# Performance work log

Measured on AMD Instinct MI355X. Metric: run time of the kernel, lower is better.

## Reference

```python
import jax, jax.numpy as jnp
import numpy as np

N_NODES = 100000
N_EDGES = 1600000
DIMS = [128, 128, 128, 64]


def setup_inputs() -> dict:
    key = jax.random.key(0)
    ks = jax.random.split(key, 12)
    inp = {
        "features": jax.random.normal(ks[0], (N_NODES, DIMS[0]), dtype=jnp.float32),
        "src": jax.random.randint(ks[1], (N_EDGES,), 0, N_NODES, dtype=jnp.int64),
        "dst": jax.random.randint(ks[2], (N_EDGES,), 0, N_NODES, dtype=jnp.int64),
        "edge_weight": jax.random.uniform(ks[3], (N_EDGES,), dtype=jnp.float32),
    }
    # GraphConv weights (xavier-like scale) and biases per layer
    for i in range(3):
        fin, fout = DIMS[i], DIMS[i + 1]
        scale = (2.0 / (fin + fout)) ** 0.5
        inp[f"W{i}"] = jax.random.normal(ks[4 + i], (fin, fout), dtype=jnp.float32) * scale
        inp[f"b{i}"] = jnp.zeros((fout,), dtype=jnp.float32)
    return inp


def _graph_conv(h, W, b, src, dst, ew, out_norm, in_norm):
    # DGL GraphConv, norm='both', with per-edge weight (u_mul_e message).
    fin, fout = W.shape
    h = h * out_norm[:, None]
    if fin > fout:  # mult W first to reduce message width
        h = h @ W
    msg = h[src] * ew[:, None]                       # [E, d] irregular gather
    agg = jax.ops.segment_sum(msg, dst, num_segments=N_NODES)
    agg = agg * in_norm[:, None]
    if fin <= fout:
        agg = agg @ W
    return agg + b


def reference(features, src, dst, edge_weight, W0, b0, W1, b1, W2, b2):
    ones = jnp.ones((N_EDGES,), dtype=features.dtype)
    out_deg = jax.ops.segment_sum(ones, src, num_segments=N_NODES)
    in_deg = jax.ops.segment_sum(ones, dst, num_segments=N_NODES)
    out_norm = jnp.clip(out_deg, 1.0, None) ** -0.5
    in_norm = jnp.clip(in_deg, 1.0, None) ** -0.5
    h = features
    Ws = [(W0, b0), (W1, b1), (W2, b2)]
    for i, (W, b) in enumerate(Ws):
        h = _graph_conv(h, W, b, src, dst, edge_weight, out_norm, in_norm)
        if i < len(Ws) - 1:
            h = jax.nn.relu(h)
    return h
```

## Files before the change

### kernel.cpp

```cpp
#include <hip/hip_runtime.h>
#include <cstddef>
#include <cstdint>

typedef float f4 __attribute__((ext_vector_type(4)));
typedef unsigned long long u64;
typedef unsigned short u16;
typedef unsigned short u16x8 __attribute__((ext_vector_type(8)));
typedef short short8 __attribute__((ext_vector_type(8)));

__device__ __forceinline__ u64 ldnt8(const void* p) {
    return __builtin_nontemporal_load((const u64*)(p));
}
__device__ __forceinline__ u16 bfrn(float f) {
    unsigned u = __float_as_uint(f);
    return (u16)((u + 0x7FFFu + ((u >> 16) & 1u)) >> 16);
}
__device__ __forceinline__ float bl(unsigned w) { return __uint_as_float(w << 16); }
__device__ __forceinline__ float bh(unsigned w) { return __uint_as_float(w & 0xFFFF0000u); }


#define EPB 4096

__global__ void __launch_bounds__(256)
k_p1(const int* __restrict__ src, const int* __restrict__ dst,
     u16* __restrict__ lrank_s, u16* __restrict__ lrank_d,
     int* __restrict__ bh_s, int* __restrict__ bh_d, int NB, int E) {
    __shared__ int hs[512], hd[512];
    const int t = threadIdx.x, b = blockIdx.x;
    for (int i = t; i < NB; i += 256) { hs[i] = 0; hd[i] = 0; }
    __syncthreads();
    const int e0 = b * EPB;
    #pragma unroll
    for (int j = 0; j < 4; ++j) {
        const int e = e0 + j * 1024 + t * 4;
        if (e + 4 <= E) {
            const int4 d = *(const int4*)&dst[e];
            const int4 s = *(const int4*)&src[e];
            unsigned rd0 = atomicAdd(&hd[d.x >> 8], 1);
            unsigned rd1 = atomicAdd(&hd[d.y >> 8], 1);
            unsigned rd2 = atomicAdd(&hd[d.z >> 8], 1);
            unsigned rd3 = atomicAdd(&hd[d.w >> 8], 1);
            unsigned rs0 = atomicAdd(&hs[s.x >> 8], 1);
            unsigned rs1 = atomicAdd(&hs[s.y >> 8], 1);
            unsigned rs2 = atomicAdd(&hs[s.z >> 8], 1);
            unsigned rs3 = atomicAdd(&hs[s.w >> 8], 1);
            *(uint2*)&lrank_d[e] = make_uint2(rd0 | (rd1 << 16), rd2 | (rd3 << 16));
            *(uint2*)&lrank_s[e] = make_uint2(rs0 | (rs1 << 16), rs2 | (rs3 << 16));
        } else {
            for (int k = e; k < E && k < e + 4; ++k) {
                lrank_d[k] = (u16)atomicAdd(&hd[dst[k] >> 8], 1);
                lrank_s[k] = (u16)atomicAdd(&hs[src[k] >> 8], 1);
            }
        }
    }
    __syncthreads();
    for (int i = t; i < NB; i += 256) {
        bh_d[b * NB + i] = hd[i];
        bh_s[b * NB + i] = hs[i];
    }
}

__global__ void __launch_bounds__(512)
k_p2(int* __restrict__ bh_d, int* __restrict__ bh_s,
     int* __restrict__ cb_d, int* __restrict__ cb_s, int NB, int B1) {
    __shared__ int s[512];
    const int B = blockIdx.x, i = threadIdx.x;
    int* bh = blockIdx.y ? bh_s : bh_d;
    int* cb = blockIdx.y ? cb_s : cb_d;
    const int v = (i < B1) ? bh[i * NB + B] : 0;
    s[i] = v;
    __syncthreads();
    for (int off = 1; off < 512; off <<= 1) {
        const int x = (i >= off) ? s[i - off] : 0;
        __syncthreads();
        s[i] += x;
        __syncthreads();
    }
    if (i < B1) bh[i * NB + B] = s[i] - v;
    if (i == 511) cb[B] = s[511];
}

__global__ void __launch_bounds__(512)
k_p2b(const int* __restrict__ cb_d, const int* __restrict__ cb_s,
      int* __restrict__ bktb_d, int* __restrict__ bktb_s,
      int* __restrict__ row, int NB, int N, int E) {
    __shared__ int s[512];
    const int t = threadIdx.x;
    int v = (t < NB) ? cb_d[t] : 0;
    s[t] = v;
    __syncthreads();
    for (int off = 1; off < 512; off <<= 1) {
        const int x = (t >= off) ? s[t - off] : 0;
        __syncthreads();
        s[t] += x;
        __syncthreads();
    }
    if (t < NB) bktb_d[t] = s[t] - v;
    __syncthreads();
    v = (t < NB) ? cb_s[t] : 0;
    s[t] = v;
    __syncthreads();
    for (int off = 1; off < 512; off <<= 1) {
        const int x = (t >= off) ? s[t - off] : 0;
        __syncthreads();
        s[t] += x;
        __syncthreads();
    }
    if (t < NB) bktb_s[t] = s[t] - v;
    if (t == 0) row[N] = E;
}

__global__ void __launch_bounds__(256)
k_p3(const int* __restrict__ src, const int* __restrict__ dst,
     const float* __restrict__ ew,
     const u16* __restrict__ lrank_s, const u16* __restrict__ lrank_d,
     const int* __restrict__ bh_s, const int* __restrict__ bh_d,
     const int* __restrict__ bktb_s, const int* __restrict__ bktb_d,
     int* __restrict__ tdst, int2* __restrict__ tsw, int* __restrict__ tsrc,
     int NB, int E) {
    const int t = threadIdx.x, b = blockIdx.x;
    const int e0 = b * EPB;
    #pragma unroll
    for (int j = 0; j < 4; ++j) {
        const int e = e0 + j * 1024 + t * 4;
        if (e + 4 <= E) {
            const int4 d = *(const int4*)&dst[e];
            const int4 s = *(const int4*)&src[e];
            const f4   w = *(const f4*)&ew[e];
            const uint2 rd = *(const uint2*)&lrank_d[e];
            const uint2 rs = *(const uint2*)&lrank_s[e];
            const int dd[4] = {d.x, d.y, d.z, d.w};
            const int ss[4] = {s.x, s.y, s.z, s.w};
            const float ww[4] = {w.x, w.y, w.z, w.w};
            const int rrd[4] = {(int)(rd.x & 0xFFFF), (int)(rd.x >> 16),
                                (int)(rd.y & 0xFFFF), (int)(rd.y >> 16)};
            const int rrs[4] = {(int)(rs.x & 0xFFFF), (int)(rs.x >> 16),
                                (int)(rs.y & 0xFFFF), (int)(rs.y >> 16)};
            #pragma unroll
            for (int k = 0; k < 4; ++k) {
                const int Bd = dd[k] >> 8;
                const int posd = bktb_d[Bd] + bh_d[b * NB + Bd] + rrd[k];
                tdst[posd] = dd[k];
                tsw[posd] = make_int2(ss[k], __float_as_int(ww[k]));
                const int Bs = ss[k] >> 8;
                const int poss = bktb_s[Bs] + bh_s[b * NB + Bs] + rrs[k];
                tsrc[poss] = ss[k];
            }
        } else {
            for (int k = e; k < E && k < e + 4; ++k) {
                const int dv = dst[k], sv = src[k];
                const int Bd = dv >> 8;
                const int posd = bktb_d[Bd] + bh_d[b * NB + Bd] + (int)lrank_d[k];
                tdst[posd] = dv;
                tsw[posd] = make_int2(sv, __float_as_int(ew[k]));
                const int Bs = sv >> 8;
                const int poss = bktb_s[Bs] + bh_s[b * NB + Bs] + (int)lrank_s[k];
                tsrc[poss] = sv;
            }
        }
    }
}

__global__ void __launch_bounds__(256)
k_p4s(const int* __restrict__ tsrc, const int* __restrict__ bktb_s,
      const int* __restrict__ cb_s, float* __restrict__ onorm, int NB, int N) {
    __shared__ int cnt[256];
    const int B = blockIdx.x, t = threadIdx.x;
    cnt[t] = 0;
    __syncthreads();
    const int base = bktb_s[B], cb = cb_s[B];
    for (int i = t; i < cb; i += 256) atomicAdd(&cnt[tsrc[base + i] & 255], 1);
    __syncthreads();
    const int n = (B << 8) + t;
    if (n < N) {
        const int c = cnt[t];
        onorm[n] = rsqrtf((float)(c < 1 ? 1 : c));
    }
}

__global__ void __launch_bounds__(256)
k_p4d(const int* __restrict__ tdst, const int2* __restrict__ tsw,
      const int* __restrict__ bktb_d, const int* __restrict__ cb_d,
      const float* __restrict__ onorm, int* __restrict__ row,
      float* __restrict__ inorm, int2* __restrict__ csr, int NB, int N) {
    __shared__ int cnt[256], cnt2[256], lrow[256], sc[256];
    const int B = blockIdx.x, t = threadIdx.x;
    cnt[t] = 0; cnt2[t] = 0;
    __syncthreads();
    const int base = bktb_d[B], cb = cb_d[B];
    for (int i = t; i < cb; i += 256) atomicAdd(&cnt[tdst[base + i] & 255], 1);
    __syncthreads();
    const int v = cnt[t];
    sc[t] = v;
    __syncthreads();
    for (int off = 1; off < 256; off <<= 1) {
        const int x = (t >= off) ? sc[t - off] : 0;
        __syncthreads();
        sc[t] += x;
        __syncthreads();
    }
    const int excl = sc[t] - v;
    lrow[t] = excl;
    const int n = (B << 8) + t;
    if (n < N) {
        row[n] = base + excl;
        inorm[n] = rsqrtf((float)(v < 1 ? 1 : v));
    }
    __syncthreads();
    for (int i = t; i < cb; i += 256) {
        const int d = tdst[base + i] & 255;
        const int2 sw = tsw[base + i];
        const int r = atomicAdd(&cnt2[d], 1);
        const float coef = __int_as_float(sw.y) * onorm[sw.x];
        csr[base + lrow[d] + r] = make_int2(sw.x, __float_as_int(coef));
    }
}

__global__ void __launch_bounds__(256)
k_cvt(const float* __restrict__ in, u16* __restrict__ out, int n8) {
    const int i = blockIdx.x * blockDim.x + threadIdx.x;
    if (i < n8) {
        const f4 v0 = *(const f4*)(in + (size_t)i * 8);
        const f4 v1 = *(const f4*)(in + (size_t)i * 8 + 4);
        u16x8 r = {bfrn(v0.x), bfrn(v0.y), bfrn(v0.z), bfrn(v0.w),
                   bfrn(v1.x), bfrn(v1.y), bfrn(v1.z), bfrn(v1.w)};
        *(u16x8*)(out + (size_t)i * 8) = r;
    }
}

template <int LOGC>
__global__ void __launch_bounds__(256)
k_wcvt(const float* __restrict__ W, u16* __restrict__ Wt, int K) {
    const int idx = blockIdx.x * 256 + threadIdx.x;
    if (idx < (K << LOGC)) {
        const int k = idx >> LOGC;
        const int c = idx & ((1 << LOGC) - 1);
        Wt[(size_t)c * K + k] = bfrn(W[idx]);
    }
}

__global__ void __launch_bounds__(256)
k_agg128b(const u16* __restrict__ h, const int* __restrict__ row,
          const int2* __restrict__ csr, const float* __restrict__ inorm,
          u16* __restrict__ out, int N) {
    const int node = (int)((blockIdx.x * blockDim.x + threadIdx.x) >> 6);
    if (node >= N) return;
    const int lane = threadIdx.x & 63;
    const int q = lane >> 4;
    const int col = (lane & 15) * 8;
    int p = row[node];
    const int e = row[node + 1];
    float a0 = 0, a1 = 0, a2 = 0, a3 = 0, a4 = 0, a5 = 0, a6 = 0, a7 = 0;
    for (; p + 16 <= e; p += 16) {
        const u64 c0 = ldnt8(&csr[p + q]);
        const u64 c1 = ldnt8(&csr[p + 4 + q]);
        const u64 c2 = ldnt8(&csr[p + 8 + q]);
        const u64 c3 = ldnt8(&csr[p + 12 + q]);
        const uint4 w0 = *(const uint4*)(h + (size_t)(int)c0 * 128 + col);
        const uint4 w1 = *(const uint4*)(h + (size_t)(int)c1 * 128 + col);
        const uint4 w2 = *(const uint4*)(h + (size_t)(int)c2 * 128 + col);
        const uint4 w3 = *(const uint4*)(h + (size_t)(int)c3 * 128 + col);
        const float f0 = __int_as_float((int)(c0 >> 32));
        const float f1 = __int_as_float((int)(c1 >> 32));
        const float f2 = __int_as_float((int)(c2 >> 32));
        const float f3 = __int_as_float((int)(c3 >> 32));
        a0 = fmaf(f0, bl(w0.x), a0); a1 = fmaf(f0, bh(w0.x), a1);
        a2 = fmaf(f0, bl(w0.y), a2); a3 = fmaf(f0, bh(w0.y), a3);
        a4 = fmaf(f0, bl(w0.z), a4); a5 = fmaf(f0, bh(w0.z), a5);
        a6 = fmaf(f0, bl(w0.w), a6); a7 = fmaf(f0, bh(w0.w), a7);
        a0 = fmaf(f1, bl(w1.x), a0); a1 = fmaf(f1, bh(w1.x), a1);
        a2 = fmaf(f1, bl(w1.y), a2); a3 = fmaf(f1, bh(w1.y), a3);
        a4 = fmaf(f1, bl(w1.z), a4); a5 = fmaf(f1, bh(w1.z), a5);
        a6 = fmaf(f1, bl(w1.w), a6); a7 = fmaf(f1, bh(w1.w), a7);
        a0 = fmaf(f2, bl(w2.x), a0); a1 = fmaf(f2, bh(w2.x), a1);
        a2 = fmaf(f2, bl(w2.y), a2); a3 = fmaf(f2, bh(w2.y), a3);
        a4 = fmaf(f2, bl(w2.z), a4); a5 = fmaf(f2, bh(w2.z), a5);
        a6 = fmaf(f2, bl(w2.w), a6); a7 = fmaf(f2, bh(w2.w), a7);
        a0 = fmaf(f3, bl(w3.x), a0); a1 = fmaf(f3, bh(w3.x), a1);
        a2 = fmaf(f3, bl(w3.y), a2); a3 = fmaf(f3, bh(w3.y), a3);
        a4 = fmaf(f3, bl(w3.z), a4); a5 = fmaf(f3, bh(w3.z), a5);
        a6 = fmaf(f3, bl(w3.w), a6); a7 = fmaf(f3, bh(w3.w), a7);
    }
    for (; p + 8 <= e; p += 8) {
        const u64 c0 = ldnt8(&csr[p + q]);
        const u64 c1 = ldnt8(&csr[p + 4 + q]);
        const uint4 w0 = *(const uint4*)(h + (size_t)(int)c0 * 128 + col);
        const uint4 w1 = *(const uint4*)(h + (size_t)(int)c1 * 128 + col);
        const float f0 = __int_as_float((int)(c0 >> 32));
        const float f1 = __int_as_float((int)(c1 >> 32));
        a0 = fmaf(f0, bl(w0.x), a0); a1 = fmaf(f0, bh(w0.x), a1);
        a2 = fmaf(f0, bl(w0.y), a2); a3 = fmaf(f0, bh(w0.y), a3);
        a4 = fmaf(f0, bl(w0.z), a4); a5 = fmaf(f0, bh(w0.z), a5);
        a6 = fmaf(f0, bl(w0.w), a6); a7 = fmaf(f0, bh(w0.w), a7);
        a0 = fmaf(f1, bl(w1.x), a0); a1 = fmaf(f1, bh(w1.x), a1);
        a2 = fmaf(f1, bl(w1.y), a2); a3 = fmaf(f1, bh(w1.y), a3);
        a4 = fmaf(f1, bl(w1.z), a4); a5 = fmaf(f1, bh(w1.z), a5);
        a6 = fmaf(f1, bl(w1.w), a6); a7 = fmaf(f1, bh(w1.w), a7);
    }
    {
        const int i0 = p + q, i1 = p + 4 + q;
        if (i0 < e) {
            const u64 c = ldnt8(&csr[i0]);
            const uint4 w = *(const uint4*)(h + (size_t)(int)c * 128 + col);
            const float f = __int_as_float((int)(c >> 32));
            a0 = fmaf(f, bl(w.x), a0); a1 = fmaf(f, bh(w.x), a1);
            a2 = fmaf(f, bl(w.y), a2); a3 = fmaf(f, bh(w.y), a3);
            a4 = fmaf(f, bl(w.z), a4); a5 = fmaf(f, bh(w.z), a5);
            a6 = fmaf(f, bl(w.w), a6); a7 = fmaf(f, bh(w.w), a7);
        }
        if (i1 < e) {
            const u64 c = ldnt8(&csr[i1]);
            const uint4 w = *(const uint4*)(h + (size_t)(int)c * 128 + col);
            const float f = __int_as_float((int)(c >> 32));
            a0 = fmaf(f, bl(w.x), a0); a1 = fmaf(f, bh(w.x), a1);
            a2 = fmaf(f, bl(w.y), a2); a3 = fmaf(f, bh(w.y), a3);
            a4 = fmaf(f, bl(w.z), a4); a5 = fmaf(f, bh(w.z), a5);
            a6 = fmaf(f, bl(w.w), a6); a7 = fmaf(f, bh(w.w), a7);
        }
    }
    a0 += __shfl_xor(a0, 16); a1 += __shfl_xor(a1, 16);
    a2 += __shfl_xor(a2, 16); a3 += __shfl_xor(a3, 16);
    a4 += __shfl_xor(a4, 16); a5 += __shfl_xor(a5, 16);
    a6 += __shfl_xor(a6, 16); a7 += __shfl_xor(a7, 16);
    a0 += __shfl_xor(a0, 32); a1 += __shfl_xor(a1, 32);
    a2 += __shfl_xor(a2, 32); a3 += __shfl_xor(a3, 32);
    a4 += __shfl_xor(a4, 32); a5 += __shfl_xor(a5, 32);
    a6 += __shfl_xor(a6, 32); a7 += __shfl_xor(a7, 32);
    if (lane < 16) {
        const float nn = inorm[node];
        u16x8 r = {bfrn(a0 * nn), bfrn(a1 * nn), bfrn(a2 * nn), bfrn(a3 * nn),
                   bfrn(a4 * nn), bfrn(a5 * nn), bfrn(a6 * nn), bfrn(a7 * nn)};
        *(u16x8*)(out + (size_t)node * 128 + col) = r;
    }
}

__global__ void __launch_bounds__(256)
k_agg64b(const u16* __restrict__ h, const int* __restrict__ row,
         const int2* __restrict__ csr, const float* __restrict__ inorm,
         const float* __restrict__ bias, float* __restrict__ out, int N) {
    const int node = (int)((blockIdx.x * blockDim.x + threadIdx.x) >> 6);
    if (node >= N) return;
    const int lane = threadIdx.x & 63;
    const int oc = lane >> 3;
    const int col = (lane & 7) * 8;
    int p = row[node];
    const int e = row[node + 1];
    float a0 = 0, a1 = 0, a2 = 0, a3 = 0, a4 = 0, a5 = 0, a6 = 0, a7 = 0;
    for (; p + 16 <= e; p += 16) {
        const u64 c0 = ldnt8(&csr[p + oc]);
        const u64 c1 = ldnt8(&csr[p + 8 + oc]);
        const uint4 w0 = *(const uint4*)(h + (size_t)(int)c0 * 64 + col);
        const uint4 w1 = *(const uint4*)(h + (size_t)(int)c1 * 64 + col);
        const float f0 = __int_as_float((int)(c0 >> 32));
        const float f1 = __int_as_float((int)(c1 >> 32));
        a0 = fmaf(f0, bl(w0.x), a0); a1 = fmaf(f0, bh(w0.x), a1);
        a2 = fmaf(f0, bl(w0.y), a2); a3 = fmaf(f0, bh(w0.y), a3);
        a4 = fmaf(f0, bl(w0.z), a4); a5 = fmaf(f0, bh(w0.z), a5);
        a6 = fmaf(f0, bl(w0.w), a6); a7 = fmaf(f0, bh(w0.w), a7);
        a0 = fmaf(f1, bl(w1.x), a0); a1 = fmaf(f1, bh(w1.x), a1);
        a2 = fmaf(f1, bl(w1.y), a2); a3 = fmaf(f1, bh(w1.y), a3);
        a4 = fmaf(f1, bl(w1.z), a4); a5 = fmaf(f1, bh(w1.z), a5);
        a6 = fmaf(f1, bl(w1.w), a6); a7 = fmaf(f1, bh(w1.w), a7);
    }
    {
        const int i0 = p + oc, i1 = p + 8 + oc;
        if (i0 < e) {
            const u64 c = ldnt8(&csr[i0]);
            const uint4 w = *(const uint4*)(h + (size_t)(int)c * 64 + col);
            const float f = __int_as_float((int)(c >> 32));
            a0 = fmaf(f, bl(w.x), a0); a1 = fmaf(f, bh(w.x), a1);
            a2 = fmaf(f, bl(w.y), a2); a3 = fmaf(f, bh(w.y), a3);
            a4 = fmaf(f, bl(w.z), a4); a5 = fmaf(f, bh(w.z), a5);
            a6 = fmaf(f, bl(w.w), a6); a7 = fmaf(f, bh(w.w), a7);
        }
        if (i1 < e) {
            const u64 c = ldnt8(&csr[i1]);
            const uint4 w = *(const uint4*)(h + (size_t)(int)c * 64 + col);
            const float f = __int_as_float((int)(c >> 32));
            a0 = fmaf(f, bl(w.x), a0); a1 = fmaf(f, bh(w.x), a1);
            a2 = fmaf(f, bl(w.y), a2); a3 = fmaf(f, bh(w.y), a3);
            a4 = fmaf(f, bl(w.z), a4); a5 = fmaf(f, bh(w.z), a5);
            a6 = fmaf(f, bl(w.w), a6); a7 = fmaf(f, bh(w.w), a7);
        }
    }
    a0 += __shfl_xor(a0, 8);  a1 += __shfl_xor(a1, 8);
    a2 += __shfl_xor(a2, 8);  a3 += __shfl_xor(a3, 8);
    a4 += __shfl_xor(a4, 8);  a5 += __shfl_xor(a5, 8);
    a6 += __shfl_xor(a6, 8);  a7 += __shfl_xor(a7, 8);
    a0 += __shfl_xor(a0, 16); a1 += __shfl_xor(a1, 16);
    a2 += __shfl_xor(a2, 16); a3 += __shfl_xor(a3, 16);
    a4 += __shfl_xor(a4, 16); a5 += __shfl_xor(a5, 16);
    a6 += __shfl_xor(a6, 16); a7 += __shfl_xor(a7, 16);
    a0 += __shfl_xor(a0, 32); a1 += __shfl_xor(a1, 32);
    a2 += __shfl_xor(a2, 32); a3 += __shfl_xor(a3, 32);
    a4 += __shfl_xor(a4, 32); a5 += __shfl_xor(a5, 32);
    a6 += __shfl_xor(a6, 32); a7 += __shfl_xor(a7, 32);
    if (lane < 8) {
        const float nn = inorm[node];
        const f4 b0 = *(const f4*)(bias + col);
        const f4 b1 = *(const f4*)(bias + col + 4);
        f4 r0 = {a0 * nn + b0.x, a1 * nn + b0.y, a2 * nn + b0.z, a3 * nn + b0.w};
        f4 r1 = {a4 * nn + b1.x, a5 * nn + b1.y, a6 * nn + b1.z, a7 * nn + b1.w};
        *(f4*)(out + (size_t)node * 64 + col) = r0;
        *(f4*)(out + (size_t)node * 64 + col + 4) = r1;
    }
}

template <int COLS, bool RELU, bool BIAS>
__global__ void __launch_bounds__(256)
k_mgemm(const u16* __restrict__ A, const u16* __restrict__ Wt,
        const float* __restrict__ bias, u16* __restrict__ C, int N) {
    __shared__ u16 Wl[COLS][136];
    const int t = threadIdx.x;
    const int lane = t & 63;
    const int wave = t >> 6;
    #pragma unroll
    for (int i = 0; i < COLS / 16; ++i) {
        const int elem = (i * 256 + t) * 8;
        const int r = elem >> 7, c0 = elem & 127;
        *(short8*)&Wl[r][c0] = *(const short8*)(Wt + elem);
    }
    const int row0 = blockIdx.x * 64 + wave * 16;
    const int arow = min(row0 + (lane & 15), N - 1);
    const int koff = (lane >> 4) * 8;
    short8 a[4];
    #pragma unroll
    for (int kk = 0; kk < 4; ++kk)
        a[kk] = *(const short8*)(A + (size_t)arow * 128 + kk * 32 + koff);
    __syncthreads();

    f4 acc[COLS / 16];
    #pragma unroll
    for (int ct = 0; ct < COLS / 16; ++ct) acc[ct] = (f4){0.f, 0.f, 0.f, 0.f};

    #pragma unroll
    for (int ct = 0; ct < COLS / 16; ++ct) {
        #pragma unroll
        for (int kk = 0; kk < 4; ++kk) {
            const short8 b = *(const short8*)&Wl[ct * 16 + (lane & 15)][kk * 32 + koff];
            acc[ct] = __builtin_amdgcn_mfma_f32_16x16x32_bf16(a[kk], b, acc[ct], 0, 0, 0);
        }
    }

    #pragma unroll
    for (int ct = 0; ct < COLS / 16; ++ct) {
        const int c = ct * 16 + (lane & 15);
        const float bb = BIAS ? bias[c] : 0.f;
        #pragma unroll
        for (int r = 0; r < 4; ++r) {
            const int gr = row0 + (lane >> 4) * 4 + r;
            if (gr < N) {
                float v = acc[ct][r] + bb;
                if (RELU) v = v > 0.f ? v : 0.f;
                C[(size_t)gr * COLS + c] = bfrn(v);
            }
        }
    }
}

extern "C" void kernel_launch(void* const* d_in, const int* in_sizes, int n_in,
                              void* d_out, int out_size, void* d_ws, size_t ws_size,
                              hipStream_t stream) {
    const float* feat = (const float*)d_in[0];
    const int*   src  = (const int*)d_in[1];
    const int*   dst  = (const int*)d_in[2];
    const float* ew   = (const float*)d_in[3];
    const float* W0   = (const float*)d_in[4];
    const float* b0   = (const float*)d_in[5];
    const float* W1   = (const float*)d_in[6];
    const float* b1   = (const float*)d_in[7];
    const float* W2   = (const float*)d_in[8];
    const float* b2   = (const float*)d_in[9];
    float* out = (float*)d_out;

    const int N = in_sizes[0] / 128;
    const int E = in_sizes[1];
    const int NB = (N + 255) / 256;
    const int B1 = (E + EPB - 1) / EPB;

    uint8_t* wp = (uint8_t*)d_ws;
    auto alloc = [&](size_t bytes) {
        uint8_t* r = wp;
        wp += (bytes + 511) & ~(size_t)511;
        return r;
    };
    u16*   featb = (u16*)alloc((size_t)N * 128 * 2);
    u16*   Xb    = (u16*)alloc((size_t)N * 128 * 2);
    u16*   Yb    = (u16*)alloc((size_t)N * 128 * 2 + 65536);
    int2*  csr   = (int2*)alloc((size_t)E * 8);
    int*   row   = (int*)alloc((size_t)(N + 1) * 4);
    float* onorm = (float*)alloc((size_t)N * 4);
    float* inorm = (float*)alloc((size_t)N * 4);
    u16*   Wt0   = (u16*)alloc(128 * 128 * 2);
    u16*   Wt1   = (u16*)alloc(128 * 128 * 2);
    u16*   Wt2   = (u16*)alloc(128 * 64 * 2);

    uint8_t* xp = (uint8_t*)Xb;
    auto xalloc = [&](size_t bytes) {
        uint8_t* r = xp;
        xp += (bytes + 511) & ~(size_t)511;
        return r;
    };
    u16* lrank_d = (u16*)xalloc((size_t)E * 2);
    u16* lrank_s = (u16*)xalloc((size_t)E * 2);
    int* bh_d    = (int*)xalloc((size_t)B1 * NB * 4);
    int* bh_s    = (int*)xalloc((size_t)B1 * NB * 4);
    int* cb_d    = (int*)xalloc((size_t)NB * 4);
    int* cb_s    = (int*)xalloc((size_t)NB * 4);
    int* bktb_d  = (int*)xalloc((size_t)NB * 4);
    int* bktb_s  = (int*)xalloc((size_t)NB * 4);

    uint8_t* yp = (uint8_t*)Yb;
    auto yalloc = [&](size_t bytes) {
        uint8_t* r = yp;
        yp += (bytes + 511) & ~(size_t)511;
        return r;
    };
    int*  tdst = (int*)yalloc((size_t)E * 4);
    int2* tsw  = (int2*)yalloc((size_t)E * 8);
    int*  tsrc = (int*)yalloc((size_t)E * 4);
    u16*  Gb   = (u16*)Yb;

    k_cvt<<<(N * 128 / 8 + 255) / 256, 256, 0, stream>>>(feat, featb, N * 128 / 8);
    k_wcvt<7><<<64, 256, 0, stream>>>(W0, Wt0, 128);
    k_wcvt<7><<<64, 256, 0, stream>>>(W1, Wt1, 128);
    k_wcvt<6><<<32, 256, 0, stream>>>(W2, Wt2, 128);
    k_p1<<<B1, 256, 0, stream>>>(src, dst, lrank_s, lrank_d, bh_s, bh_d, NB, E);
    k_p2<<<dim3(NB, 2), 512, 0, stream>>>(bh_d, bh_s, cb_d, cb_s, NB, B1);
    k_p2b<<<1, 512, 0, stream>>>(cb_d, cb_s, bktb_d, bktb_s, row, NB, N, E);
    k_p3<<<B1, 256, 0, stream>>>(src, dst, ew, lrank_s, lrank_d, bh_s, bh_d,
                                 bktb_s, bktb_d, tdst, tsw, tsrc, NB, E);
    k_p4s<<<NB, 256, 0, stream>>>(tsrc, bktb_s, cb_s, onorm, NB, N);
    k_p4d<<<NB, 256, 0, stream>>>(tdst, tsw, bktb_d, cb_d, onorm, row, inorm,
                                  csr, NB, N);

    const int ab = (N + 3) / 4;
    const int gb = (N + 63) / 64;

    k_agg128b<<<ab, 256, 0, stream>>>(featb, row, csr, inorm, Yb, N);
    k_mgemm<128, true, true><<<gb, 256, 0, stream>>>(Yb, Wt0, b0, Xb, N);
    k_agg128b<<<ab, 256, 0, stream>>>(Xb, row, csr, inorm, Yb, N);
    k_mgemm<128, true, true><<<gb, 256, 0, stream>>>(Yb, Wt1, b1, Xb, N);
    k_mgemm<64, false, false><<<gb, 256, 0, stream>>>(Xb, Wt2, nullptr, Gb, N);
    k_agg64b<<<ab, 256, 0, stream>>>(Gb, row, csr, inorm, b2, out, N);
}
```

Measured before the change: 338.7 us.

## Recompute local ranks in scatter pass and pack dst byte into src word

The histogram pass no longer writes per-edge local ranks. The scatter pass recomputes them with shared-memory atomics and caches bucket bases in shared memory. The separate tdst array is dropped by packing the low byte of dst into the top 8 bits of the src index in tsw, and tsrc shrinks from int to one byte. The three weight-conversion kernels are merged into one launch, and the workspace buffers are reassigned. This cuts global traffic and launch count, but relies on atomic rank order within a block matching the order in k_p1 only in counts, and it assumes node ids fit in 24 bits.

```diff
diff --git a/kernel.cpp b/kernel.cpp
--- a/kernel.cpp
+++ b/kernel.cpp
@@ -5,6 +5,7 @@
 typedef float f4 __attribute__((ext_vector_type(4)));
 typedef unsigned long long u64;
 typedef unsigned short u16;
+typedef unsigned char u8;
 typedef unsigned short u16x8 __attribute__((ext_vector_type(8)));
 typedef short short8 __attribute__((ext_vector_type(8)));
 
@@ -23,11 +24,10 @@
 
 __global__ void __launch_bounds__(256)
 k_p1(const int* __restrict__ src, const int* __restrict__ dst,
-     u16* __restrict__ lrank_s, u16* __restrict__ lrank_d,
      int* __restrict__ bh_s, int* __restrict__ bh_d, int NB, int E) {
     __shared__ int hs[512], hd[512];
     const int t = threadIdx.x, b = blockIdx.x;
-    for (int i = t; i < NB; i += 256) { hs[i] = 0; hd[i] = 0; }
+    for (int i = t; i < 512; i += 256) { hs[i] = 0; hd[i] = 0; }
     __syncthreads();
     const int e0 = b * EPB;
     #pragma unroll
@@ -36,20 +36,18 @@
         if (e + 4 <= E) {
             const int4 d = *(const int4*)&dst[e];
             const int4 s = *(const int4*)&src[e];
-            unsigned rd0 = atomicAdd(&hd[d.x >> 8], 1);
-            unsigned rd1 = atomicAdd(&hd[d.y >> 8], 1);
-            unsigned rd2 = atomicAdd(&hd[d.z >> 8], 1);
-            unsigned rd3 = atomicAdd(&hd[d.w >> 8], 1);
-            unsigned rs0 = atomicAdd(&hs[s.x >> 8], 1);
-            unsigned rs1 = atomicAdd(&hs[s.y >> 8], 1);
-            unsigned rs2 = atomicAdd(&hs[s.z >> 8], 1);
-            unsigned rs3 = atomicAdd(&hs[s.w >> 8], 1);
-            *(uint2*)&lrank_d[e] = make_uint2(rd0 | (rd1 << 16), rd2 | (rd3 << 16));
-            *(uint2*)&lrank_s[e] = make_uint2(rs0 | (rs1 << 16), rs2 | (rs3 << 16));
+            atomicAdd(&hd[d.x >> 8], 1);
+            atomicAdd(&hd[d.y >> 8], 1);
+            atomicAdd(&hd[d.z >> 8], 1);
+            atomicAdd(&hd[d.w >> 8], 1);
+            atomicAdd(&hs[s.x >> 8], 1);
+            atomicAdd(&hs[s.y >> 8], 1);
+            atomicAdd(&hs[s.z >> 8], 1);
+            atomicAdd(&hs[s.w >> 8], 1);
         } else {
             for (int k = e; k < E && k < e + 4; ++k) {
-                lrank_d[k] = (u16)atomicAdd(&hd[dst[k] >> 8], 1);
-                lrank_s[k] = (u16)atomicAdd(&hs[src[k] >> 8], 1);
+                atomicAdd(&hd[dst[k] >> 8], 1);
+                atomicAdd(&hs[src[k] >> 8], 1);
             }
         }
     }
@@ -113,12 +111,19 @@
 __global__ void __launch_bounds__(256)
 k_p3(const int* __restrict__ src, const int* __restrict__ dst,
      const float* __restrict__ ew,
-     const u16* __restrict__ lrank_s, const u16* __restrict__ lrank_d,
      const int* __restrict__ bh_s, const int* __restrict__ bh_d,
      const int* __restrict__ bktb_s, const int* __restrict__ bktb_d,
-     int* __restrict__ tdst, int2* __restrict__ tsw, int* __restrict__ tsrc,
-     int NB, int E) {
+     int2* __restrict__ tsw, u8* __restrict__ tsrc, int NB, int E) {
+    __shared__ int hs[512], hd[512], base_s[512], base_d[512];
     const int t = threadIdx.x, b = blockIdx.x;
+    for (int i = t; i < 512; i += 256) {
+        hs[i] = 0; hd[i] = 0;
+        if (i < NB) {
+            base_d[i] = bktb_d[i] + bh_d[b * NB + i];
+            base_s[i] = bktb_s[i] + bh_s[b * NB + i];
+        }
+    }
+    __syncthreads();
     const int e0 = b * EPB;
     #pragma unroll
     for (int j = 0; j < 4; ++j) {
@@ -127,49 +132,43 @@
             const int4 d = *(const int4*)&dst[e];
             const int4 s = *(const int4*)&src[e];
             const f4   w = *(const f4*)&ew[e];
-            const uint2 rd = *(const uint2*)&lrank_d[e];
-            const uint2 rs = *(const uint2*)&lrank_s[e];
             const int dd[4] = {d.x, d.y, d.z, d.w};
             const int ss[4] = {s.x, s.y, s.z, s.w};
             const float ww[4] = {w.x, w.y, w.z, w.w};
-            const int rrd[4] = {(int)(rd.x & 0xFFFF), (int)(rd.x >> 16),
-                                (int)(rd.y & 0xFFFF), (int)(rd.y >> 16)};
-            const int rrs[4] = {(int)(rs.x & 0xFFFF), (int)(rs.x >> 16),
-                                (int)(rs.y & 0xFFFF), (int)(rs.y >> 16)};
             #pragma unroll
             for (int k = 0; k < 4; ++k) {
                 const int Bd = dd[k] >> 8;
-                const int posd = bktb_d[Bd] + bh_d[b * NB + Bd] + rrd[k];
-                tdst[posd] = dd[k];
-                tsw[posd] = make_int2(ss[k], __float_as_int(ww[k]));
+                const int rd = atomicAdd(&hd[Bd], 1);
+                tsw[base_d[Bd] + rd] = make_int2(ss[k] | ((dd[k] & 255) << 24),
+                                                 __float_as_int(ww[k]));
                 const int Bs = ss[k] >> 8;
-                const int poss = bktb_s[Bs] + bh_s[b * NB + Bs] + rrs[k];
-                tsrc[poss] = ss[k];
+                const int rs = atomicAdd(&hs[Bs], 1);
+                tsrc[base_s[Bs] + rs] = (u8)(ss[k] & 255);
             }
         } else {
             for (int k = e; k < E && k < e + 4; ++k) {
                 const int dv = dst[k], sv = src[k];
                 const int Bd = dv >> 8;
-                const int posd = bktb_d[Bd] + bh_d[b * NB + Bd] + (int)lrank_d[k];
-                tdst[posd] = dv;
-                tsw[posd] = make_int2(sv, __float_as_int(ew[k]));
+                const int rd = atomicAdd(&hd[Bd], 1);
+                tsw[base_d[Bd] + rd] = make_int2(sv | ((dv & 255) << 24),
+                                                 __float_as_int(ew[k]));
                 const int Bs = sv >> 8;
-                const int poss = bktb_s[Bs] + bh_s[b * NB + Bs] + (int)lrank_s[k];
-                tsrc[poss] = sv;
+                const int rs = atomicAdd(&hs[Bs], 1);
+                tsrc[base_s[Bs] + rs] = (u8)(sv & 255);
             }
         }
     }
 }
 
 __global__ void __launch_bounds__(256)
-k_p4s(const int* __restrict__ tsrc, const int* __restrict__ bktb_s,
+k_p4s(const u8* __restrict__ tsrc, const int* __restrict__ bktb_s,
       const int* __restrict__ cb_s, float* __restrict__ onorm, int NB, int N) {
     __shared__ int cnt[256];
     const int B = blockIdx.x, t = threadIdx.x;
     cnt[t] = 0;
     __syncthreads();
     const int base = bktb_s[B], cb = cb_s[B];
-    for (int i = t; i < cb; i += 256) atomicAdd(&cnt[tsrc[base + i] & 255], 1);
+    for (int i = t; i < cb; i += 256) atomicAdd(&cnt[tsrc[base + i]], 1);
     __syncthreads();
     const int n = (B << 8) + t;
     if (n < N) {
@@ -179,7 +178,7 @@
 }
 
 __global__ void __launch_bounds__(256)
-k_p4d(const int* __restrict__ tdst, const int2* __restrict__ tsw,
+k_p4d(const int2* __restrict__ tsw,
       const int* __restrict__ bktb_d, const int* __restrict__ cb_d,
       const float* __restrict__ onorm, int* __restrict__ row,
       float* __restrict__ inorm, int2* __restrict__ csr, int NB, int N) {
@@ -188,7 +187,8 @@
     cnt[t] = 0; cnt2[t] = 0;
     __syncthreads();
     const int base = bktb_d[B], cb = cb_d[B];
-    for (int i = t; i < cb; i += 256) atomicAdd(&cnt[tdst[base + i] & 255], 1);
+    for (int i = t; i < cb; i += 256)
+        atomicAdd(&cnt[((unsigned)tsw[base + i].x) >> 24], 1);
     __syncthreads();
     const int v = cnt[t];
     sc[t] = v;
@@ -208,11 +208,12 @@
     }
     __syncthreads();
     for (int i = t; i < cb; i += 256) {
-        const int d = tdst[base + i] & 255;
         const int2 sw = tsw[base + i];
+        const int d = ((unsigned)sw.x) >> 24;
+        const int s = sw.x & 0xFFFFFF;
         const int r = atomicAdd(&cnt2[d], 1);
-        const float coef = __int_as_float(sw.y) * onorm[sw.x];
-        csr[base + lrow[d] + r] = make_int2(sw.x, __float_as_int(coef));
+        const float coef = __int_as_float(sw.y) * onorm[s];
+        csr[base + lrow[d] + r] = make_int2(s, __float_as_int(coef));
     }
 }
 
@@ -228,14 +229,20 @@
     }
 }
 
-template <int LOGC>
-__global__ void __launch_bounds__(256)
-k_wcvt(const float* __restrict__ W, u16* __restrict__ Wt, int K) {
-    const int idx = blockIdx.x * 256 + threadIdx.x;
-    if (idx < (K << LOGC)) {
-        const int k = idx >> LOGC;
-        const int c = idx & ((1 << LOGC) - 1);
-        Wt[(size_t)c * K + k] = bfrn(W[idx]);
+__global__ void __launch_bounds__(256)
+k_wcvt3(const float* __restrict__ W0, const float* __restrict__ W1,
+        const float* __restrict__ W2, u16* __restrict__ Wt0,
+        u16* __restrict__ Wt1, u16* __restrict__ Wt2) {
+    const int i = blockIdx.x * 256 + threadIdx.x;
+    if (i < 16384) {
+        const int k = i >> 7, c = i & 127;
+        Wt0[c * 128 + k] = bfrn(W0[i]);
+    } else if (i < 32768) {
+        const int j = i - 16384, k = j >> 7, c = j & 127;
+        Wt1[c * 128 + k] = bfrn(W1[j]);
+    } else if (i < 40960) {
+        const int j = i - 32768, k = j >> 6, c = j & 63;
+        Wt2[c * 128 + k] = bfrn(W2[j]);
     }
 }
 
@@ -486,7 +493,8 @@
     };
     u16*   featb = (u16*)alloc((size_t)N * 128 * 2);
     u16*   Xb    = (u16*)alloc((size_t)N * 128 * 2);
-    u16*   Yb    = (u16*)alloc((size_t)N * 128 * 2 + 65536);
+    u16*   Tb    = (u16*)alloc((size_t)N * 128 * 2);
+    u8*    scr   = (u8*)alloc((size_t)E * 10 + 65536);
     int2*  csr   = (int2*)alloc((size_t)E * 8);
     int*   row   = (int*)alloc((size_t)(N + 1) * 4);
     float* onorm = (float*)alloc((size_t)N * 4);
@@ -501,46 +509,40 @@
         xp += (bytes + 511) & ~(size_t)511;
         return r;
     };
-    u16* lrank_d = (u16*)xalloc((size_t)E * 2);
-    u16* lrank_s = (u16*)xalloc((size_t)E * 2);
-    int* bh_d    = (int*)xalloc((size_t)B1 * NB * 4);
-    int* bh_s    = (int*)xalloc((size_t)B1 * NB * 4);
-    int* cb_d    = (int*)xalloc((size_t)NB * 4);
-    int* cb_s    = (int*)xalloc((size_t)NB * 4);
-    int* bktb_d  = (int*)xalloc((size_t)NB * 4);
-    int* bktb_s  = (int*)xalloc((size_t)NB * 4);
-
-    uint8_t* yp = (uint8_t*)Yb;
+    int* bh_d   = (int*)xalloc((size_t)B1 * NB * 4);
+    int* bh_s   = (int*)xalloc((size_t)B1 * NB * 4);
+    int* cb_d   = (int*)xalloc((size_t)NB * 4);
+    int* cb_s   = (int*)xalloc((size_t)NB * 4);
+    int* bktb_d = (int*)xalloc((size_t)NB * 4);
+    int* bktb_s = (int*)xalloc((size_t)NB * 4);
+
+    uint8_t* yp = scr;
     auto yalloc = [&](size_t bytes) {
         uint8_t* r = yp;
         yp += (bytes + 511) & ~(size_t)511;
         return r;
     };
-    int*  tdst = (int*)yalloc((size_t)E * 4);
     int2* tsw  = (int2*)yalloc((size_t)E * 8);
-    int*  tsrc = (int*)yalloc((size_t)E * 4);
-    u16*  Gb   = (u16*)Yb;
+    u8*   tsrc = (u8*)yalloc((size_t)E);
+    u16*  Gb   = (u16*)scr;
 
     k_cvt<<<(N * 128 / 8 + 255) / 256, 256, 0, stream>>>(feat, featb, N * 128 / 8);
-    k_wcvt<7><<<64, 256, 0, stream>>>(W0, Wt0, 128);
-    k_wcvt<7><<<64, 256, 0, stream>>>(W1, Wt1, 128);
-    k_wcvt<6><<<32, 256, 0, stream>>>(W2, Wt2, 128);
-    k_p1<<<B1, 256, 0, stream>>>(src, dst, lrank_s, lrank_d, bh_s, bh_d, NB, E);
+    k_wcvt3<<<160, 256, 0, stream>>>(W0, W1, W2, Wt0, Wt1, Wt2);
+    k_p1<<<B1, 256, 0, stream>>>(src, dst, bh_s, bh_d, NB, E);
     k_p2<<<dim3(NB, 2), 512, 0, stream>>>(bh_d, bh_s, cb_d, cb_s, NB, B1);
     k_p2b<<<1, 512, 0, stream>>>(cb_d, cb_s, bktb_d, bktb_s, row, NB, N, E);
-    k_p3<<<B1, 256, 0, stream>>>(src, dst, ew, lrank_s, lrank_d, bh_s, bh_d,
-                                 bktb_s, bktb_d, tdst, tsw, tsrc, NB, E);
+    k_p3<<<B1, 256, 0, stream>>>(src, dst, ew, bh_s, bh_d, bktb_s, bktb_d,
+                                 tsw, tsrc, NB, E);
     k_p4s<<<NB, 256, 0, stream>>>(tsrc, bktb_s, cb_s, onorm, NB, N);
-    k_p4d<<<NB, 256, 0, stream>>>(tdst, tsw, bktb_d, cb_d, onorm, row, inorm,
-                                  csr, NB, N);
+    k_p4d<<<NB, 256, 0, stream>>>(tsw, bktb_d, cb_d, onorm, row, inorm, csr, NB, N);
 
     const int ab = (N + 3) / 4;
     const int gb = (N + 63) / 64;
 
-    k_agg128b<<<ab, 256, 0, stream>>>(featb, row, csr, inorm, Yb, N);
-    k_mgemm<128, true, true><<<gb, 256, 0, stream>>>(Yb, Wt0, b0, Xb, N);
-    k_agg128b<<<ab, 256, 0, stream>>>(Xb, row, csr, inorm, Yb, N);
-    k_mgemm<128, true, true><<<gb, 256, 0, stream>>>(Yb, Wt1, b1, Xb, N);
-    k_mgemm<64, false, false><<<gb, 256, 0, stream>>>(Xb, Wt2, nullptr, Gb, N);
+    k_agg128b<<<ab, 256, 0, stream>>>(featb, row, csr, inorm, Tb, N);
+    k_mgemm<128, true, true><<<gb, 256, 0, stream>>>(Tb, Wt0, b0, Xb, N);
+    k_agg128b<<<ab, 256, 0, stream>>>(Xb, row, csr, inorm, Tb, N);
+    k_mgemm<128, true, true><<<gb, 256, 0, stream>>>(Tb, Wt1, b1, featb, N);
+    k_mgemm<64, false, false><<<gb, 256, 0, stream>>>(featb, Wt2, nullptr, Gb, N);
     k_agg64b<<<ab, 256, 0, stream>>>(Gb, row, csr, inorm, b2, out, N);
 }
```

New measurement: 313.4 us. 7.5% less time.
